# Optimization experiments

Hardware: AMD Instinct MI355X
Metric: run time of the kernel (lower is better)

The kernel has to match this reference:

```python
import jax, jax.numpy as jnp
import numpy as np

B, N, C, H, W = 4, 262144, 40, 256, 256
HID = 128


def _bilinear_sample(plane, u, v):
    """torch F.grid_sample(mode='bilinear', padding_mode='zeros', align_corners=False).
    plane: (B, C, H, W); u, v: (B, N) in [-1, 1] (u -> width axis, v -> height axis).
    Returns (B, N, C)."""
    Wd, Hd = plane.shape[3], plane.shape[2]
    ix = ((u + 1.0) * Wd - 1.0) * 0.5
    iy = ((v + 1.0) * Hd - 1.0) * 0.5
    ix0 = jnp.floor(ix)
    iy0 = jnp.floor(iy)
    fx = ix - ix0
    fy = iy - iy0
    ix0 = ix0.astype(jnp.int32)
    iy0 = iy0.astype(jnp.int32)
    flat = plane.reshape(plane.shape[0], plane.shape[1], Hd * Wd)  # (B,C,H*W)

    def corner(xi, yi, w):
        valid = (xi >= 0) & (xi < Wd) & (yi >= 0) & (yi < Hd)
        xc = jnp.clip(xi, 0, Wd - 1)
        yc = jnp.clip(yi, 0, Hd - 1)
        idx = yc * Wd + xc  # (B,N)
        vals = jnp.take_along_axis(flat, idx[:, None, :], axis=2)  # (B,C,N)
        return vals * (w * valid)[:, None, :]

    out = (corner(ix0, iy0, (1 - fx) * (1 - fy))
           + corner(ix0 + 1, iy0, fx * (1 - fy))
           + corner(ix0, iy0 + 1, (1 - fx) * fy)
           + corner(ix0 + 1, iy0 + 1, fx * fy))  # (B,C,N)
    return jnp.transpose(out, (0, 2, 1))  # (B,N,C)


def _sample_triplane(triplane, coords):
    x, y, z = coords[..., 0], coords[..., 1], coords[..., 2]
    f_xy = _bilinear_sample(triplane[:, 0], x, y)
    f_xz = _bilinear_sample(triplane[:, 1], x, z)
    f_yz = _bilinear_sample(triplane[:, 2], y, z)
    return jnp.concatenate([f_xy, f_xz, f_yz], axis=-1)  # (B,N,3C)


def setup_inputs() -> dict:
    key = jax.random.key(0)
    ks = jax.random.split(key, 16)
    triplane = jax.random.normal(ks[0], (B, 3, C, H, W), dtype=jnp.float32)
    coords = jax.random.uniform(ks[1], (B, N, 3), dtype=jnp.float32) * 2.0 - 1.0
    vd = jax.random.normal(ks[2], (B, N, 3), dtype=jnp.float32)
    view_dirs = vd / (jnp.linalg.norm(vd, axis=-1, keepdims=True) + 1e-8)
    s = 0.05
    p = {
        'triplane': triplane, 'coords': coords, 'view_dirs': view_dirs,
        'dw1': jax.random.normal(ks[3], (3 * C, HID), dtype=jnp.float32) * s,
        'db1': jnp.zeros((HID,), jnp.float32),
        'dw2': jax.random.normal(ks[4], (HID, HID), dtype=jnp.float32) * s,
        'db2': jnp.zeros((HID,), jnp.float32),
        'dw3': jax.random.normal(ks[5], (HID, 1), dtype=jnp.float32) * s,
        'db3': jnp.zeros((1,), jnp.float32),
        'cw1': jax.random.normal(ks[6], (3 * C + 3, HID), dtype=jnp.float32) * s,
        'cb1': jnp.zeros((HID,), jnp.float32),
        'cw2': jax.random.normal(ks[7], (HID, HID), dtype=jnp.float32) * s,
        'cb2': jnp.zeros((HID,), jnp.float32),
        'cw3': jax.random.normal(ks[8], (HID, 3), dtype=jnp.float32) * s,
        'cb3': jnp.zeros((3,), jnp.float32),
    }
    return p


def reference(triplane, coords, view_dirs, dw1, db1, dw2, db2, dw3, db3,
              cw1, cb1, cw2, cb2, cw3, cb3):
    feats = _sample_triplane(triplane, coords)  # (B,N,3C)
    h = jax.nn.relu(feats @ dw1 + db1)
    h = jax.nn.relu(h @ dw2 + db2)
    density = h @ dw3 + db3  # (B,N,1)
    cin = jnp.concatenate([feats, view_dirs], axis=-1)
    g = jax.nn.relu(cin @ cw1 + cb1)
    g = jax.nn.relu(g @ cw2 + cb2)
    rgb = jax.nn.sigmoid(g @ cw3 + cb3)  # (B,N,3)
    return density, rgb
```

## Files before the change

### kernel.cpp

```cpp
#include <hip/hip_runtime.h>
#include <cstdint>
#include <cstddef>

typedef __bf16 bf16x8 __attribute__((ext_vector_type(8)));
typedef float  f32x4  __attribute__((ext_vector_type(4)));

#define MFMA16(a,b,c) __builtin_amdgcn_mfma_f32_16x16x32_bf16((a),(b),(c),0,0,0)

__device__ __forceinline__ uint f2bf1(float f){
  uint u = __builtin_bit_cast(uint, f);
  u += 0x7FFFu + ((u >> 16) & 1u);
  return u >> 16;
}
__device__ __forceinline__ uint pack2(float a, float b){
  return f2bf1(a) | (f2bf1(b) << 16);
}
__device__ __forceinline__ uint pack2f(float a, float b){
  uint ua = __builtin_bit_cast(uint, a) + 0x8000u;
  uint ub = __builtin_bit_cast(uint, b) + 0x8000u;
  return __builtin_amdgcn_perm(ub, ua, 0x07060302u);
}
__device__ __forceinline__ float bflo(uint d){ return __builtin_bit_cast(float, d << 16); }
__device__ __forceinline__ float bfhi(uint d){ return __builtin_bit_cast(float, d & 0xFFFF0000u); }

__global__ __launch_bounds__(256, 4) void prep_k(
    const float* __restrict__ tri, ushort* __restrict__ tp,
    const float* __restrict__ dw1, const float* __restrict__ cw1,
    const float* __restrict__ dw2, const float* __restrict__ cw2,
    const float* __restrict__ dw3, const float* __restrict__ cw3,
    uint4* __restrict__ wpk)
{
  __shared__ uint stu[40 * 130];
  const int tid = threadIdx.x;
  if (blockIdx.x < 3072){
    const int y = blockIdx.x & 255;
    const int q = blockIdx.x >> 8;
    const float* src = tri + (size_t)q * 40 * 65536 + y * 256;
#pragma unroll
    for (int it = 0; it < 10; it++){
      int lin = it * 256 + tid;
      int c = lin >> 6, xq = lin & 63;
      const float4 v = *(const float4*)(src + (size_t)c * 65536 + xq * 4);
      uint2 w; w.x = pack2(v.x, v.y); w.y = pack2(v.z, v.w);
      *(uint2*)&stu[c * 130 + 2 * xq] = w;
    }
    __syncthreads();
    uint4* dst = (uint4*)(tp + ((size_t)q * 65536 + (size_t)y * 256) * 40);
#pragma unroll
    for (int it = 0; it < 5; it++){
      int m = it * 256 + tid;
      uint4 o;
#pragma unroll
      for (int jj = 0; jj < 4; jj++){
        int d  = 4 * m + jj;
        int x  = (d * 3277) >> 16;
        int cp = d - x * 20;
        uint A = stu[(2 * cp    ) * 130 + (x >> 1)];
        uint B = stu[(2 * cp + 1) * 130 + (x >> 1)];
        ((uint*)&o)[jj] = (x & 1) ? ((A >> 16)      | (B & 0xFFFF0000u))
                                  : ((A & 0xFFFFu)  | (B << 16));
      }
      dst[m] = o;
    }
  } else {
    int idx = (blockIdx.x - 3072) * 256 + tid;
    if (idx >= 8704) return;
    int mode, rel;
    if      (idx < 2048){ mode = 0; rel = idx; }
    else if (idx < 4096){ mode = 1; rel = idx - 2048; }
    else if (idx < 6144){ mode = 2; rel = idx - 4096; }
    else if (idx < 8192){ mode = 3; rel = idx - 6144; }
    else if (idx < 8448){ mode = 4; rel = idx - 8192; }
    else                { mode = 5; rel = idx - 8448; }
    int frag = rel >> 6, lane = rel & 63;
    int Mt = frag >> 2, s = frag & 3;
    int m  = Mt * 16 + (lane & 15);
    int kb = s * 32 + (lane >> 4) * 8;
    uint d[4];
#pragma unroll
    for (int jj = 0; jj < 4; jj++){
      float v0 = 0.f, v1 = 0.f;
#pragma unroll
      for (int h = 0; h < 2; h++){
        int k = kb + jj * 2 + h;
        float v = 0.f;
        switch (mode){
          case 0: v = (k < 120) ? dw1[k * 128 + m] : 0.f; break;
          case 1: v = (k < 123) ? cw1[k * 128 + m] : 0.f; break;
          case 2: v = dw2[k * 128 + m]; break;
          case 3: v = cw2[k * 128 + m]; break;
          case 4: v = (m == 0) ? dw3[k] : 0.f; break;
          default: v = (m >= 1 && m <= 3) ? cw3[k * 3 + (m - 1)] : 0.f; break;
        }
        if (h == 0) v0 = v; else v1 = v;
      }
      d[jj] = pack2(v0, v1);
    }
    uint4 o; o.x = d[0]; o.y = d[1]; o.z = d[2]; o.w = d[3];
    wpk[idx] = o;
  }
}

__device__ __forceinline__ uint4 blend4(uint4 a, uint4 b, uint4 c, uint4 d,
                                        float w00, float w10, float w01, float w11){
  uint4 ov;
  ov.x = pack2f(w00*bflo(a.x)+w10*bflo(b.x)+w01*bflo(c.x)+w11*bflo(d.x),
                w00*bfhi(a.x)+w10*bfhi(b.x)+w01*bfhi(c.x)+w11*bfhi(d.x));
  ov.y = pack2f(w00*bflo(a.y)+w10*bflo(b.y)+w01*bflo(c.y)+w11*bflo(d.y),
                w00*bfhi(a.y)+w10*bfhi(b.y)+w01*bfhi(c.y)+w11*bfhi(d.y));
  ov.z = pack2f(w00*bflo(a.z)+w10*bflo(b.z)+w01*bflo(c.z)+w11*bflo(d.z),
                w00*bfhi(a.z)+w10*bfhi(b.z)+w01*bfhi(c.z)+w11*bfhi(d.z));
  ov.w = pack2f(w00*bflo(a.w)+w10*bflo(b.w)+w01*bflo(c.w)+w11*bflo(d.w),
                w00*bfhi(a.w)+w10*bfhi(b.w)+w01*bfhi(c.w)+w11*bfhi(d.w));
  return ov;
}

__device__ __forceinline__ bf16x8 read_h(const uint* S, int s, int t, int lrow, int lq){
  int dwb = (s * 16 + lq * 4 + (lrow << 2)) & 63;
  return __builtin_bit_cast(bf16x8, *(const uint4*)&S[(t * 16 + lrow) * 64 + dwb]);
}

__device__ __forceinline__ void put_h(uint* S, f32x4 v, int Mt, int t, int lrow, int lq){
  uint2 w;
  w.x = pack2f(fmaxf(v[0], 0.f), fmaxf(v[1], 0.f));
  w.y = pack2f(fmaxf(v[2], 0.f), fmaxf(v[3], 0.f));
  int dw = (Mt * 8 + lq * 2 + (lrow << 2)) & 63;
  *(uint2*)&S[(t * 16 + lrow) * 64 + dw] = w;
}

__device__ __forceinline__ void layer1(uint* S, const uint4* __restrict__ W,
                                       const float* __restrict__ bias,
                                       const uint4 (&bf)[4][2],
                                       int lrow, int lq, int lane){
#pragma unroll
  for (int half = 0; half < 2; half++){
    f32x4 acc[4][2];
#pragma unroll
    for (int mt = 0; mt < 4; mt++){
      f32x4 bi = *(const f32x4*)(bias + (half * 4 + mt) * 16 + lq * 4);
      acc[mt][0] = bi; acc[mt][1] = bi;
    }
#pragma unroll
    for (int s = 0; s < 4; s++)
#pragma unroll
      for (int mt = 0; mt < 4; mt++){
        bf16x8 aw = __builtin_bit_cast(bf16x8, W[((half * 4 + mt) * 4 + s) * 64 + lane]);
        acc[mt][0] = MFMA16(aw, __builtin_bit_cast(bf16x8, bf[s][0]), acc[mt][0]);
        acc[mt][1] = MFMA16(aw, __builtin_bit_cast(bf16x8, bf[s][1]), acc[mt][1]);
      }
#pragma unroll
    for (int mt = 0; mt < 4; mt++){
      put_h(S, acc[mt][0], half * 4 + mt, 0, lrow, lq);
      put_h(S, acc[mt][1], half * 4 + mt, 1, lrow, lq);
    }
  }
}

__device__ __forceinline__ void dense_l(uint* S, const uint4* __restrict__ W,
                                        const float* __restrict__ bias,
                                        int lrow, int lq, int lane){
  bf16x8 hb[4][2];
#pragma unroll
  for (int s = 0; s < 4; s++){
    hb[s][0] = read_h(S, s, 0, lrow, lq);
    hb[s][1] = read_h(S, s, 1, lrow, lq);
  }
#pragma unroll
  for (int half = 0; half < 2; half++){
    f32x4 acc[4][2];
#pragma unroll
    for (int mt = 0; mt < 4; mt++){
      f32x4 bi = *(const f32x4*)(bias + (half * 4 + mt) * 16 + lq * 4);
      acc[mt][0] = bi; acc[mt][1] = bi;
    }
#pragma unroll
    for (int s = 0; s < 4; s++)
#pragma unroll
      for (int mt = 0; mt < 4; mt++){
        bf16x8 aw = __builtin_bit_cast(bf16x8, W[((half * 4 + mt) * 4 + s) * 64 + lane]);
        acc[mt][0] = MFMA16(aw, hb[s][0], acc[mt][0]);
        acc[mt][1] = MFMA16(aw, hb[s][1], acc[mt][1]);
      }
#pragma unroll
    for (int mt = 0; mt < 4; mt++){
      put_h(S, acc[mt][0], half * 4 + mt, 0, lrow, lq);
      put_h(S, acc[mt][1], half * 4 + mt, 1, lrow, lq);
    }
  }
}

__device__ __forceinline__ void out_l(const uint* S, const uint4* __restrict__ W,
                                      f32x4 (&acc3)[2], int lrow, int lq, int lane){
#pragma unroll
  for (int s = 0; s < 4; s++){
    bf16x8 aw = __builtin_bit_cast(bf16x8, W[s * 64 + lane]);
    acc3[0] = MFMA16(aw, read_h(S, s, 0, lrow, lq), acc3[0]);
    acc3[1] = MFMA16(aw, read_h(S, s, 1, lrow, lq), acc3[1]);
  }
}

__global__ __launch_bounds__(256, 3) void fused_k(
    const ushort* __restrict__ tp, const float* __restrict__ coords,
    const float* __restrict__ vdirs, const uint4* __restrict__ wpk,
    const float* __restrict__ db1, const float* __restrict__ db2,
    const float* __restrict__ db3, const float* __restrict__ cb1,
    const float* __restrict__ cb2, const float* __restrict__ cb3,
    float* __restrict__ out)
{
  __shared__ uint smem[4][2048];
  const int wave = threadIdx.x >> 6;
  uint* S = smem[wave];
  const int lane = threadIdx.x & 63, lrow = lane & 15, lq = lane >> 4;
  const int blk   = blockIdx.x;
  const int pbase = (blk & 3) * 262144 + (blk >> 2) * 128 + wave * 32;

  uint4 bf[4][2];
#pragma unroll
  for (int t = 0; t < 2; t++){
    const int p  = pbase + t * 16 + lrow;
    const int bb = p >> 18;
    const float cx = coords[3 * p], cy = coords[3 * p + 1], cz = coords[3 * p + 2];
    float pw00[3], pw10[3], pw01[3], pw11[3];
    uint  o00[3], o10[3], o01[3], o11[3];
#pragma unroll
    for (int pl = 0; pl < 3; pl++){
      const float u = (pl == 2) ? cy : cx;
      const float v = (pl == 0) ? cy : cz;
      float ix = fmaf(u, 128.f, 127.5f);
      float iy = fmaf(v, 128.f, 127.5f);
      float fx0 = floorf(ix), fy0 = floorf(iy);
      float fx = ix - fx0, fy = iy - fy0;
      int x0 = (int)fx0, y0 = (int)fy0;
      float wx0 = (x0 >= 0  && x0 < 256) ? (1.f - fx) : 0.f;
      float wx1 = (x0 >= -1 && x0 < 255) ? fx : 0.f;
      float wy0 = (y0 >= 0  && y0 < 256) ? (1.f - fy) : 0.f;
      float wy1 = (y0 >= -1 && y0 < 255) ? fy : 0.f;
      int xc0 = min(max(x0, 0), 255), xc1 = min(max(x0 + 1, 0), 255);
      int yc0 = min(max(y0, 0), 255), yc1 = min(max(y0 + 1, 0), 255);
      pw00[pl] = wx0 * wy0; pw10[pl] = wx1 * wy0;
      pw01[pl] = wx0 * wy1; pw11[pl] = wx1 * wy1;
      o00[pl] = ((uint)yc0 * 256u + (uint)xc0) * 40u;
      o10[pl] = ((uint)yc0 * 256u + (uint)xc1) * 40u;
      o01[pl] = ((uint)yc1 * 256u + (uint)xc0) * 40u;
      o11[pl] = ((uint)yc1 * 256u + (uint)xc1) * 40u;
    }
#pragma unroll
    for (int s = 0; s < 4; s++){
      const int chunk = s * 4 + lq;
      if (chunk == 15){
        const float v0 = vdirs[3 * p], v1 = vdirs[3 * p + 1], v2 = vdirs[3 * p + 2];
        uint4 tt; tt.x = pack2f(v0, v1); tt.y = pack2f(v2, 0.f); tt.z = 0u; tt.w = 0u;
        bf[s][t] = tt;
      } else {
        const int pl = (chunk < 5) ? 0 : (chunk < 10) ? 1 : 2;
        const int c0 = chunk * 8 - pl * 40;
        const ushort* base = tp + (size_t)(bb * 3 + pl) * 2621440 + c0;
        uint4 a = *(const uint4*)(base + o00[pl]);
        uint4 b = *(const uint4*)(base + o10[pl]);
        uint4 c = *(const uint4*)(base + o01[pl]);
        uint4 d = *(const uint4*)(base + o11[pl]);
        bf[s][t] = blend4(a, b, c, d, pw00[pl], pw10[pl], pw01[pl], pw11[pl]);
      }
    }
  }

  layer1 (S, wpk,        db1, bf, lrow, lq, lane);
  dense_l(S, wpk + 4096, db2,     lrow, lq, lane);

  f32x4 acc3[2];
  {
    float i0 = (lq == 0) ? db3[0] : 0.f;
    float i1 = (lq == 0) ? cb3[0] : 0.f;
    float i2 = (lq == 0) ? cb3[1] : 0.f;
    float i3 = (lq == 0) ? cb3[2] : 0.f;
    f32x4 iv = {i0, i1, i2, i3};
    acc3[0] = iv; acc3[1] = iv;
  }
  out_l  (S, wpk + 8192, acc3,    lrow, lq, lane);
  layer1 (S, wpk + 2048, cb1, bf, lrow, lq, lane);
  dense_l(S, wpk + 6144, cb2,     lrow, lq, lane);
  out_l  (S, wpk + 8448, acc3,    lrow, lq, lane);

  if (lq == 0){
#pragma unroll
    for (int t = 0; t < 2; t++){
      int p = pbase + t * 16 + lrow;
      out[p] = acc3[t][0];
      float* rgb = out + 1048576 + (size_t)p * 3;
      rgb[0] = 1.f / (1.f + __expf(-acc3[t][1]));
      rgb[1] = 1.f / (1.f + __expf(-acc3[t][2]));
      rgb[2] = 1.f / (1.f + __expf(-acc3[t][3]));
    }
  }
}

extern "C" void kernel_launch(void* const* d_in, const int* in_sizes, int n_in,
                              void* d_out, int out_size, void* d_ws, size_t ws_size,
                              hipStream_t stream)
{
  (void)in_sizes; (void)n_in; (void)out_size; (void)ws_size;
  const float* tri    = (const float*)d_in[0];
  const float* coords = (const float*)d_in[1];
  const float* vdirs  = (const float*)d_in[2];
  const float* dw1 = (const float*)d_in[3];  const float* db1 = (const float*)d_in[4];
  const float* dw2 = (const float*)d_in[5];  const float* db2 = (const float*)d_in[6];
  const float* dw3 = (const float*)d_in[7];  const float* db3 = (const float*)d_in[8];
  const float* cw1 = (const float*)d_in[9];  const float* cb1 = (const float*)d_in[10];
  const float* cw2 = (const float*)d_in[11]; const float* cb2 = (const float*)d_in[12];
  const float* cw3 = (const float*)d_in[13]; const float* cb3 = (const float*)d_in[14];

  char* ws = (char*)d_ws;
  const size_t planes_bytes = 62914560;
  ushort* tp  = (ushort*)ws;
  uint4*  wpk = (uint4*)(ws + planes_bytes);

  prep_k<<<3106, 256, 0, stream>>>(tri, tp, dw1, cw1, dw2, cw2, dw3, cw3, wpk);
  fused_k<<<8192, 256, 0, stream>>>(tp, coords, vdirs, wpk,
                                    db1, db2, db3, cb1, cb2, cb3,
                                    (float*)d_out);
}
```

Before: 722.1 us.

## Split fused gather+MLP kernel into per-batch gather and MLP kernels

The single fused kernel is split into a gather kernel, which samples the triplane and writes bf16 features to a workspace buffer, and an MLP kernel, which reads those features back. The work is launched per batch segment so each segment's feature buffer can stay resident in L2/LLC. Separating the stages lets each kernel run at higher occupancy (launch bounds 4 instead of 3) and removes the need to hold the gathered features in registers across both MLPs. The cost is extra global write and read traffic for the features plus eight kernel launches instead of one.

```diff
diff --git a/kernel.cpp b/kernel.cpp
--- a/kernel.cpp
+++ b/kernel.cpp
@@ -199,26 +199,19 @@
   }
 }
 
-__global__ __launch_bounds__(256, 3) void fused_k(
+__global__ __launch_bounds__(256, 4) void gather_k(
     const ushort* __restrict__ tp, const float* __restrict__ coords,
-    const float* __restrict__ vdirs, const uint4* __restrict__ wpk,
-    const float* __restrict__ db1, const float* __restrict__ db2,
-    const float* __restrict__ db3, const float* __restrict__ cb1,
-    const float* __restrict__ cb2, const float* __restrict__ cb3,
-    float* __restrict__ out)
+    const float* __restrict__ vdirs, uint4* __restrict__ feats, int seg)
 {
-  __shared__ uint smem[4][2048];
-  const int wave = threadIdx.x >> 6;
-  uint* S = smem[wave];
   const int lane = threadIdx.x & 63, lrow = lane & 15, lq = lane >> 4;
-  const int blk   = blockIdx.x;
-  const int pbase = (blk & 3) * 262144 + (blk >> 2) * 128 + wave * 32;
+  const int tile = blockIdx.x * 4 + (threadIdx.x >> 6);
+  const int pbase = seg * 262144 + tile * 32;
+  const int bb = seg;
 
   uint4 bf[4][2];
 #pragma unroll
   for (int t = 0; t < 2; t++){
     const int p  = pbase + t * 16 + lrow;
-    const int bb = p >> 18;
     const float cx = coords[3 * p], cy = coords[3 * p + 1], cz = coords[3 * p + 2];
     float pw00[3], pw10[3], pw01[3], pw11[3];
     uint  o00[3], o10[3], o01[3], o11[3];
@@ -264,8 +257,39 @@
     }
   }
 
-  layer1 (S, wpk,        db1, bf, lrow, lq, lane);
-  dense_l(S, wpk + 4096, db2,     lrow, lq, lane);
+  uint4* fb = feats + ((size_t)tile * 8) * 64 + lane;
+#pragma unroll
+  for (int s = 0; s < 4; s++)
+#pragma unroll
+    for (int t = 0; t < 2; t++)
+      fb[(s * 2 + t) * 64] = bf[s][t];
+}
+
+__global__ __launch_bounds__(256, 4) void mlp_k(
+    const uint4* __restrict__ feats, const uint4* __restrict__ wpk,
+    const float* __restrict__ db1, const float* __restrict__ db2,
+    const float* __restrict__ db3, const float* __restrict__ cb1,
+    const float* __restrict__ cb2, const float* __restrict__ cb3,
+    float* __restrict__ out, int seg)
+{
+  __shared__ uint smem[4][2048];
+  const int wave = threadIdx.x >> 6;
+  uint* S = smem[wave];
+  const int lane = threadIdx.x & 63, lrow = lane & 15, lq = lane >> 4;
+  const int tile = blockIdx.x * 4 + wave;
+  const int pbase = seg * 262144 + tile * 32;
+
+  {
+    const uint4* fb = feats + ((size_t)tile * 8) * 64 + lane;
+    uint4 bf[4][2];
+#pragma unroll
+    for (int s = 0; s < 4; s++)
+#pragma unroll
+      for (int t = 0; t < 2; t++)
+        bf[s][t] = fb[(s * 2 + t) * 64];
+    layer1(S, wpk, db1, bf, lrow, lq, lane);
+  }
+  dense_l(S, wpk + 4096, db2, lrow, lq, lane);
 
   f32x4 acc3[2];
   {
@@ -276,10 +300,22 @@
     f32x4 iv = {i0, i1, i2, i3};
     acc3[0] = iv; acc3[1] = iv;
   }
-  out_l  (S, wpk + 8192, acc3,    lrow, lq, lane);
-  layer1 (S, wpk + 2048, cb1, bf, lrow, lq, lane);
-  dense_l(S, wpk + 6144, cb2,     lrow, lq, lane);
-  out_l  (S, wpk + 8448, acc3,    lrow, lq, lane);
+  out_l(S, wpk + 8192, acc3, lrow, lq, lane);
+
+  {
+    uint tb = (uint)(tile * 8);
+    asm volatile("" : "+v"(tb));
+    const uint4* fb2 = feats + (size_t)tb * 64 + lane;
+    uint4 bf[4][2];
+#pragma unroll
+    for (int s = 0; s < 4; s++)
+#pragma unroll
+      for (int t = 0; t < 2; t++)
+        bf[s][t] = fb2[(s * 2 + t) * 64];
+    layer1(S, wpk + 2048, cb1, bf, lrow, lq, lane);
+  }
+  dense_l(S, wpk + 6144, cb2, lrow, lq, lane);
+  out_l(S, wpk + 8448, acc3, lrow, lq, lane);
 
   if (lq == 0){
 #pragma unroll
@@ -311,11 +347,15 @@
 
   char* ws = (char*)d_ws;
   const size_t planes_bytes = 62914560;
-  ushort* tp  = (ushort*)ws;
-  uint4*  wpk = (uint4*)(ws + planes_bytes);
+  const size_t wpk_bytes    = 139264;
+  ushort* tp    = (ushort*)ws;
+  uint4*  wpk   = (uint4*)(ws + planes_bytes);
+  uint4*  feats = (uint4*)(ws + planes_bytes + wpk_bytes);
 
   prep_k<<<3106, 256, 0, stream>>>(tri, tp, dw1, cw1, dw2, cw2, dw3, cw3, wpk);
-  fused_k<<<8192, 256, 0, stream>>>(tp, coords, vdirs, wpk,
-                                    db1, db2, db3, cb1, cb2, cb3,
-                                    (float*)d_out);
-}
+  for (int seg = 0; seg < 4; ++seg){
+    gather_k<<<2048, 256, 0, stream>>>(tp, coords, vdirs, feats, seg);
+    mlp_k<<<2048, 256, 0, stream>>>(feats, wpk, db1, db2, db3,
+                                    cb1, cb2, cb3, (float*)d_out, seg);
+  }
+}
```

New measurement: 899.2 us. +24.5%, slower.

## Double-buffer MLP weights in LDS via async global_load_lds staging

Applied to the files above, without the earlier changes.

Weights that each wave used to read straight from global memory (via cache) are now staged cooperatively into two LDS buffers of 16 KB each with global_load_lds. The next weight chunk is prefetched while the current half-layer runs its MFMAs, and block-wide barriers separate the stages. Launch bounds drop from 3 to 2 blocks per SM because of the extra 32 KB of LDS. The aim is to cut redundant per-wave global weight traffic. The cost is lower occupancy to hide the gather latency, plus ten __syncthreads. Barriers placed right after an async LDS load may also not wait for that load to land unless a vmcnt wait is inserted.

```diff
diff --git a/kernel.cpp b/kernel.cpp
--- a/kernel.cpp
+++ b/kernel.cpp
@@ -128,68 +128,75 @@
   *(uint2*)&S[(t * 16 + lrow) * 64 + dw] = w;
 }
 
-__device__ __forceinline__ void layer1(uint* S, const uint4* __restrict__ W,
-                                       const float* __restrict__ bias,
-                                       const uint4 (&bf)[4][2],
-                                       int lrow, int lq, int lane){
-#pragma unroll
-  for (int half = 0; half < 2; half++){
-    f32x4 acc[4][2];
+__device__ __forceinline__ void stage16(const uint4* __restrict__ g, uint4* l,
+                                        int wave, int lane, int nchunk){
+  for (int c = wave; c < nchunk; c += 4){
+    __builtin_amdgcn_global_load_lds(
+      (const __attribute__((address_space(1))) void*)(g + c * 64 + lane),
+      (__attribute__((address_space(3))) void*)(l + c * 64 + lane), 16, 0, 0);
+  }
+}
+
+__device__ __forceinline__ void layer1_half(uint* S, const uint4* W,
+                                            const float* __restrict__ bias,
+                                            const uint4 (&bf)[4][2], int half,
+                                            int lrow, int lq, int lane){
+  f32x4 acc[4][2];
+#pragma unroll
+  for (int mt = 0; mt < 4; mt++){
+    f32x4 bi = *(const f32x4*)(bias + (half * 4 + mt) * 16 + lq * 4);
+    acc[mt][0] = bi; acc[mt][1] = bi;
+  }
+#pragma unroll
+  for (int s = 0; s < 4; s++)
 #pragma unroll
     for (int mt = 0; mt < 4; mt++){
-      f32x4 bi = *(const f32x4*)(bias + (half * 4 + mt) * 16 + lq * 4);
-      acc[mt][0] = bi; acc[mt][1] = bi;
-    }
-#pragma unroll
-    for (int s = 0; s < 4; s++)
-#pragma unroll
-      for (int mt = 0; mt < 4; mt++){
-        bf16x8 aw = __builtin_bit_cast(bf16x8, W[((half * 4 + mt) * 4 + s) * 64 + lane]);
-        acc[mt][0] = MFMA16(aw, __builtin_bit_cast(bf16x8, bf[s][0]), acc[mt][0]);
-        acc[mt][1] = MFMA16(aw, __builtin_bit_cast(bf16x8, bf[s][1]), acc[mt][1]);
-      }
-#pragma unroll
-    for (int mt = 0; mt < 4; mt++){
-      put_h(S, acc[mt][0], half * 4 + mt, 0, lrow, lq);
-      put_h(S, acc[mt][1], half * 4 + mt, 1, lrow, lq);
-    }
-  }
-}
-
-__device__ __forceinline__ void dense_l(uint* S, const uint4* __restrict__ W,
-                                        const float* __restrict__ bias,
-                                        int lrow, int lq, int lane){
-  bf16x8 hb[4][2];
+      bf16x8 aw = __builtin_bit_cast(bf16x8, W[(mt * 4 + s) * 64 + lane]);
+      acc[mt][0] = MFMA16(aw, __builtin_bit_cast(bf16x8, bf[s][0]), acc[mt][0]);
+      acc[mt][1] = MFMA16(aw, __builtin_bit_cast(bf16x8, bf[s][1]), acc[mt][1]);
+    }
+#pragma unroll
+  for (int mt = 0; mt < 4; mt++){
+    put_h(S, acc[mt][0], half * 4 + mt, 0, lrow, lq);
+    put_h(S, acc[mt][1], half * 4 + mt, 1, lrow, lq);
+  }
+}
+
+__device__ __forceinline__ void load_hb(const uint* S, bf16x8 (&hb)[4][2],
+                                        int lrow, int lq){
 #pragma unroll
   for (int s = 0; s < 4; s++){
     hb[s][0] = read_h(S, s, 0, lrow, lq);
     hb[s][1] = read_h(S, s, 1, lrow, lq);
   }
-#pragma unroll
-  for (int half = 0; half < 2; half++){
-    f32x4 acc[4][2];
+}
+
+__device__ __forceinline__ void dense_half(uint* S, const uint4* W,
+                                           const float* __restrict__ bias,
+                                           const bf16x8 (&hb)[4][2], int half,
+                                           int lrow, int lq, int lane){
+  f32x4 acc[4][2];
+#pragma unroll
+  for (int mt = 0; mt < 4; mt++){
+    f32x4 bi = *(const f32x4*)(bias + (half * 4 + mt) * 16 + lq * 4);
+    acc[mt][0] = bi; acc[mt][1] = bi;
+  }
+#pragma unroll
+  for (int s = 0; s < 4; s++)
 #pragma unroll
     for (int mt = 0; mt < 4; mt++){
-      f32x4 bi = *(const f32x4*)(bias + (half * 4 + mt) * 16 + lq * 4);
-      acc[mt][0] = bi; acc[mt][1] = bi;
-    }
-#pragma unroll
-    for (int s = 0; s < 4; s++)
-#pragma unroll
-      for (int mt = 0; mt < 4; mt++){
-        bf16x8 aw = __builtin_bit_cast(bf16x8, W[((half * 4 + mt) * 4 + s) * 64 + lane]);
-        acc[mt][0] = MFMA16(aw, hb[s][0], acc[mt][0]);
-        acc[mt][1] = MFMA16(aw, hb[s][1], acc[mt][1]);
-      }
-#pragma unroll
-    for (int mt = 0; mt < 4; mt++){
-      put_h(S, acc[mt][0], half * 4 + mt, 0, lrow, lq);
-      put_h(S, acc[mt][1], half * 4 + mt, 1, lrow, lq);
-    }
-  }
-}
-
-__device__ __forceinline__ void out_l(const uint* S, const uint4* __restrict__ W,
+      bf16x8 aw = __builtin_bit_cast(bf16x8, W[(mt * 4 + s) * 64 + lane]);
+      acc[mt][0] = MFMA16(aw, hb[s][0], acc[mt][0]);
+      acc[mt][1] = MFMA16(aw, hb[s][1], acc[mt][1]);
+    }
+#pragma unroll
+  for (int mt = 0; mt < 4; mt++){
+    put_h(S, acc[mt][0], half * 4 + mt, 0, lrow, lq);
+    put_h(S, acc[mt][1], half * 4 + mt, 1, lrow, lq);
+  }
+}
+
+__device__ __forceinline__ void out_l(const uint* S, const uint4* W,
                                       f32x4 (&acc3)[2], int lrow, int lq, int lane){
 #pragma unroll
   for (int s = 0; s < 4; s++){
@@ -199,7 +206,7 @@
   }
 }
 
-__global__ __launch_bounds__(256, 3) void fused_k(
+__global__ __launch_bounds__(256, 2) void fused_k(
     const ushort* __restrict__ tp, const float* __restrict__ coords,
     const float* __restrict__ vdirs, const uint4* __restrict__ wpk,
     const float* __restrict__ db1, const float* __restrict__ db2,
@@ -207,12 +214,15 @@
     const float* __restrict__ cb2, const float* __restrict__ cb3,
     float* __restrict__ out)
 {
-  __shared__ uint smem[4][2048];
+  __shared__ uint  Sh[4][2048];
+  __shared__ uint4 WB[2][1024];
   const int wave = threadIdx.x >> 6;
-  uint* S = smem[wave];
+  uint* S = Sh[wave];
   const int lane = threadIdx.x & 63, lrow = lane & 15, lq = lane >> 4;
   const int blk   = blockIdx.x;
   const int pbase = (blk & 3) * 262144 + (blk >> 2) * 128 + wave * 32;
+
+  stage16(wpk + 0, WB[0], wave, lane, 16);
 
   uint4 bf[4][2];
 #pragma unroll
@@ -264,9 +274,6 @@
     }
   }
 
-  layer1 (S, wpk,        db1, bf, lrow, lq, lane);
-  dense_l(S, wpk + 4096, db2,     lrow, lq, lane);
-
   f32x4 acc3[2];
   {
     float i0 = (lq == 0) ? db3[0] : 0.f;
@@ -276,10 +283,40 @@
     f32x4 iv = {i0, i1, i2, i3};
     acc3[0] = iv; acc3[1] = iv;
   }
-  out_l  (S, wpk + 8192, acc3,    lrow, lq, lane);
-  layer1 (S, wpk + 2048, cb1, bf, lrow, lq, lane);
-  dense_l(S, wpk + 6144, cb2,     lrow, lq, lane);
-  out_l  (S, wpk + 8448, acc3,    lrow, lq, lane);
+
+  __syncthreads();
+  stage16(wpk + 1024, WB[1], wave, lane, 16);
+  layer1_half(S, WB[0], db1, bf, 0, lrow, lq, lane);
+  __syncthreads();
+  stage16(wpk + 4096, WB[0], wave, lane, 16);
+  layer1_half(S, WB[1], db1, bf, 1, lrow, lq, lane);
+  __syncthreads();
+  stage16(wpk + 5120, WB[1], wave, lane, 16);
+  bf16x8 hb[4][2];
+  load_hb(S, hb, lrow, lq);
+  dense_half(S, WB[0], db2, hb, 0, lrow, lq, lane);
+  __syncthreads();
+  stage16(wpk + 8192, WB[0], wave, lane, 4);
+  dense_half(S, WB[1], db2, hb, 1, lrow, lq, lane);
+  __syncthreads();
+  stage16(wpk + 2048, WB[1], wave, lane, 16);
+  out_l(S, WB[0], acc3, lrow, lq, lane);
+  __syncthreads();
+  stage16(wpk + 3072, WB[0], wave, lane, 16);
+  layer1_half(S, WB[1], cb1, bf, 0, lrow, lq, lane);
+  __syncthreads();
+  stage16(wpk + 6144, WB[1], wave, lane, 16);
+  layer1_half(S, WB[0], cb1, bf, 1, lrow, lq, lane);
+  __syncthreads();
+  stage16(wpk + 7168, WB[0], wave, lane, 16);
+  bf16x8 hb2[4][2];
+  load_hb(S, hb2, lrow, lq);
+  dense_half(S, WB[1], cb2, hb2, 0, lrow, lq, lane);
+  __syncthreads();
+  stage16(wpk + 8448, WB[1], wave, lane, 4);
+  dense_half(S, WB[0], cb2, hb2, 1, lrow, lq, lane);
+  __syncthreads();
+  out_l(S, WB[1], acc3, lrow, lq, lane);
 
   if (lq == 0){
 #pragma unroll
```

After: 580.7 us. -19.6%, faster.
